# Performance work log

Hardware: AMD Instinct MI355X
Metric: run time of the kernel (lower is better)

Reference implementation:

```python
import jax, jax.numpy as jnp
import numpy as np


def _dense_image_warp(image, flow):
    """Faithful port of tfa.image.dense_image_warp (bilinear, edge-clamped).

    output[b, y, x, c] = image[b, y - flow[b,y,x,0], x - flow[b,y,x,1], c]
    with bilinear interpolation; floor indices clipped to [0, size-2] and
    alphas clipped to [0, 1], matching TFA's interpolate_bilinear.
    """
    B, H, W, C = image.shape
    gy = jnp.arange(H, dtype=flow.dtype)[None, :, None]  # [1,H,1]
    gx = jnp.arange(W, dtype=flow.dtype)[None, None, :]  # [1,1,W]
    qy = gy - flow[..., 0]  # [B,H,W] query y coords
    qx = gx - flow[..., 1]  # [B,H,W] query x coords

    y0f = jnp.clip(jnp.floor(qy), 0.0, H - 2)
    x0f = jnp.clip(jnp.floor(qx), 0.0, W - 2)
    ay = jnp.clip(qy - y0f, 0.0, 1.0)[..., None]  # [B,H,W,1]
    ax = jnp.clip(qx - x0f, 0.0, 1.0)[..., None]
    y0 = y0f.astype(jnp.int32)
    x0 = x0f.astype(jnp.int32)
    y1 = y0 + 1
    x1 = x0 + 1

    b_idx = jnp.arange(B, dtype=jnp.int32)[:, None, None]  # [B,1,1]
    tl = image[b_idx, y0, x0]  # [B,H,W,C]
    tr = image[b_idx, y0, x1]
    bl = image[b_idx, y1, x0]
    br = image[b_idx, y1, x1]

    top = tl + ax * (tr - tl)
    bot = bl + ax * (br - bl)
    return top + ay * (bot - top)


def setup_inputs() -> dict:
    key = jax.random.key(0)
    k0, k1, k2, k3 = jax.random.split(key, 4)
    B, H, W = 16, 512, 512
    return {
        "frame_0": jax.random.uniform(k0, (B, H, W, 3), dtype=jnp.float32),
        "frame_1": jax.random.uniform(k1, (B, H, W, 3), dtype=jnp.float32),
        "f_01": jax.random.normal(k2, (B, H, W, 2), dtype=jnp.float32),
        "f_10": jax.random.normal(k3, (B, H, W, 2), dtype=jnp.float32),
    }


def reference(frame_0, frame_1, f_01, f_10):
    # WarpingOutput: [backwarp(frame_0, f_10), backwarp(frame_1, f_01)]
    return (_dense_image_warp(frame_0, f_10), _dense_image_warp(frame_1, f_01))
```

## Files before the change

kernel.cpp:

```cpp
#include <hip/hip_runtime.h>

#define BB 16
#define HH 512
#define WW 512
#define TH 16
#define TW 64
#define HALO 8
#define SR 33
#define SC 80
#define ROWQ (SC / 4)
#define NUNIT (SR * ROWQ)
#define NPIX (BB * HH * WW)

typedef float vf4 __attribute__((ext_vector_type(4)));
typedef unsigned int u32;
typedef u32 vu4 __attribute__((ext_vector_type(4)));
typedef u32 vu2 __attribute__((ext_vector_type(2)));

__device__ __forceinline__ u32 cvt_pk_bf16(float lo, float hi) {
    u32 r;
    asm("v_cvt_pk_bf16_f32 %0, %1, %2" : "=v"(r) : "v"(lo), "v"(hi));
    return r;
}
__device__ __forceinline__ float bf_lo(u32 w) { return __uint_as_float(w << 16); }
__device__ __forceinline__ float bf_hi(u32 w) { return __uint_as_float(w & 0xffff0000u); }

__global__ __launch_bounds__(256, 7) void warp2_kernel(
    const float* __restrict__ frame0,
    const float* __restrict__ frame1,
    const float* __restrict__ f01,
    const float* __restrict__ f10,
    float* __restrict__ out)
{
    __shared__ vu2 plds[SR * SC];

    const int bid = blockIdx.x;
    const int gt  = (bid & 7) * 1024 + (bid >> 3);
    const int which = gt >> 12;
    const int b     = (gt >> 8) & 15;
    const int tt    = gt & 255;
    const int ty    = (tt >> 3) * TH;
    const int tx    = (tt & 7) * TW;

    const float* __restrict__ img  = which ? frame1 : frame0;
    const float* __restrict__ flow = which ? f01    : f10;

    const int r0 = min(max(ty - HALO, 0), HH - SR);
    const int c0 = min(max(tx - HALO, 0), WW - SC);

    const int tid = threadIdx.x;

    const int r  = tid >> 4;
    const int q  = tid & 15;
    const int y  = ty + r;
    const int xq = tx + (q << 2);
    const size_t pixbase = (size_t)(b * HH + y) * WW + xq;
    const vf4 fl0 = __builtin_nontemporal_load(reinterpret_cast<const vf4*>(flow + 2 * pixbase));
    const vf4 fl1 = __builtin_nontemporal_load(reinterpret_cast<const vf4*>(flow + 2 * pixbase + 4));

    #pragma unroll
    for (int it = 0; it < 3; ++it) {
        const int s = tid + (it << 8);
        if (it < 2 || s < NUNIT) {
            const int row = s / ROWQ;
            const int u   = s - row * ROWQ;
            const float* g = img + ((size_t)((b * HH + r0 + row) * WW + c0 + (u << 2))) * 3;
            const vf4 a0 = *reinterpret_cast<const vf4*>(g);
            const vf4 a1 = *reinterpret_cast<const vf4*>(g + 4);
            const vf4 a2 = *reinterpret_cast<const vf4*>(g + 8);
            const vu4 w0 = { cvt_pk_bf16(a0.x, a0.y), cvt_pk_bf16(a0.z, 0.0f),
                             cvt_pk_bf16(a0.w, a1.x), cvt_pk_bf16(a1.y, 0.0f) };
            const vu4 w1 = { cvt_pk_bf16(a1.z, a1.w), cvt_pk_bf16(a2.x, 0.0f),
                             cvt_pk_bf16(a2.y, a2.z), cvt_pk_bf16(a2.w, 0.0f) };
            const int base = row * SC + (u << 2);
            *reinterpret_cast<vu4*>(&plds[base])     = w0;
            *reinterpret_cast<vu4*>(&plds[base + 2]) = w1;
        }
    }
    __syncthreads();

    float res[12];
    #pragma unroll
    for (int s = 0; s < 4; ++s) {
        const float dy = (s == 0) ? fl0.x : (s == 1) ? fl0.z : (s == 2) ? fl1.x : fl1.z;
        const float dx = (s == 0) ? fl0.y : (s == 1) ? fl0.w : (s == 2) ? fl1.y : fl1.w;
        const int xs = xq + s;

        const float qy = (float)y  - dy;
        const float qx = (float)xs - dx;
        const float y0f = fminf(fmaxf(floorf(qy), 0.0f), (float)(HH - 2));
        const float x0f = fminf(fmaxf(floorf(qx), 0.0f), (float)(WW - 2));
        const float ay = fminf(fmaxf(qy - y0f, 0.0f), 1.0f);
        const float ax = fminf(fmaxf(qx - x0f, 0.0f), 1.0f);
        const int y0 = (int)y0f;
        const int x0 = (int)x0f;

        float tl0, tl1, tl2, tr0, tr1, tr2, bl0, bl1, bl2, br0, br1, br2;
        if (y0 >= r0 && y0 < r0 + SR - 1 && x0 >= c0 && x0 < c0 + SC - 1) {
            const int o = (y0 - r0) * SC + (x0 - c0);
            const vu2 tl = plds[o];      const vu2 tr = plds[o + 1];
            const vu2 bl = plds[o + SC]; const vu2 br = plds[o + SC + 1];
            tl0 = bf_lo(tl.x); tl1 = bf_hi(tl.x); tl2 = bf_lo(tl.y);
            tr0 = bf_lo(tr.x); tr1 = bf_hi(tr.x); tr2 = bf_lo(tr.y);
            bl0 = bf_lo(bl.x); bl1 = bf_hi(bl.x); bl2 = bf_lo(bl.y);
            br0 = bf_lo(br.x); br1 = bf_hi(br.x); br2 = bf_lo(br.y);
        } else {
            const float* rowt = img + ((size_t)((b * HH + y0) * WW + x0)) * 3;
            const float* rowb = rowt + WW * 3;
            const float3 tl = *reinterpret_cast<const float3*>(rowt);
            const float3 tr = *reinterpret_cast<const float3*>(rowt + 3);
            const float3 bl = *reinterpret_cast<const float3*>(rowb);
            const float3 br = *reinterpret_cast<const float3*>(rowb + 3);
            tl0 = tl.x; tl1 = tl.y; tl2 = tl.z;
            tr0 = tr.x; tr1 = tr.y; tr2 = tr.z;
            bl0 = bl.x; bl1 = bl.y; bl2 = bl.z;
            br0 = br.x; br1 = br.y; br2 = br.z;
        }

        const float t0 = fmaf(ax, tr0 - tl0, tl0);
        const float t1 = fmaf(ax, tr1 - tl1, tl1);
        const float t2 = fmaf(ax, tr2 - tl2, tl2);
        const float q0 = fmaf(ax, br0 - bl0, bl0);
        const float q1 = fmaf(ax, br1 - bl1, bl1);
        const float q2 = fmaf(ax, br2 - bl2, bl2);
        res[3 * s + 0] = fmaf(ay, q0 - t0, t0);
        res[3 * s + 1] = fmaf(ay, q1 - t1, t1);
        res[3 * s + 2] = fmaf(ay, q2 - t2, t2);
    }

    float* o = out + 3 * (((size_t)which) * NPIX + pixbase);
    const vf4 s0 = {res[0], res[1], res[2],  res[3]};
    const vf4 s1 = {res[4], res[5], res[6],  res[7]};
    const vf4 s2 = {res[8], res[9], res[10], res[11]};
    *reinterpret_cast<vf4*>(o)     = s0;
    *reinterpret_cast<vf4*>(o + 4) = s1;
    *reinterpret_cast<vf4*>(o + 8) = s2;
}

extern "C" void kernel_launch(void* const* d_in, const int* in_sizes, int n_in,
                              void* d_out, int out_size, void* d_ws, size_t ws_size,
                              hipStream_t stream) {
    const float* frame0 = (const float*)d_in[0];
    const float* frame1 = (const float*)d_in[1];
    const float* f01    = (const float*)d_in[2];
    const float* f10    = (const float*)d_in[3];
    float* out = (float*)d_out;

    warp2_kernel<<<8192, 256, 0, stream>>>(frame0, frame1, f01, f10, out);
}
```

Before: 57.45 us.

## Double tile height, 8 pixels per thread, pad LDS stride

Doubles the output tile height to 32 rows so the staged halo region (49x80) is amortized over more output pixels. Each thread now handles 8 pixels, halving the block count. The shared-memory row stride is padded to 81 to reduce bank conflicts, which forces the staging stores to be split into four 8-byte writes. Occupancy hint drops to 5 blocks per CU because of the larger LDS footprint and register use.

```diff
diff --git a/kernel.cpp b/kernel.cpp
--- a/kernel.cpp
+++ b/kernel.cpp
@@ -3,18 +3,18 @@
 #define BB 16
 #define HH 512
 #define WW 512
-#define TH 16
+#define TH 32
 #define TW 64
 #define HALO 8
-#define SR 33
+#define SR 49
 #define SC 80
+#define SSTRIDE 81
 #define ROWQ (SC / 4)
 #define NUNIT (SR * ROWQ)
 #define NPIX (BB * HH * WW)
 
 typedef float vf4 __attribute__((ext_vector_type(4)));
 typedef unsigned int u32;
-typedef u32 vu4 __attribute__((ext_vector_type(4)));
 typedef u32 vu2 __attribute__((ext_vector_type(2)));
 
 __device__ __forceinline__ u32 cvt_pk_bf16(float lo, float hi) {
@@ -25,20 +25,20 @@
 __device__ __forceinline__ float bf_lo(u32 w) { return __uint_as_float(w << 16); }
 __device__ __forceinline__ float bf_hi(u32 w) { return __uint_as_float(w & 0xffff0000u); }
 
-__global__ __launch_bounds__(256, 7) void warp2_kernel(
+__global__ __launch_bounds__(256, 5) void warp2_kernel(
     const float* __restrict__ frame0,
     const float* __restrict__ frame1,
     const float* __restrict__ f01,
     const float* __restrict__ f10,
     float* __restrict__ out)
 {
-    __shared__ vu2 plds[SR * SC];
+    __shared__ vu2 plds[SR * SSTRIDE];
 
     const int bid = blockIdx.x;
-    const int gt  = (bid & 7) * 1024 + (bid >> 3);
-    const int which = gt >> 12;
-    const int b     = (gt >> 8) & 15;
-    const int tt    = gt & 255;
+    const int gt  = (bid & 7) * 512 + (bid >> 3);
+    const int which = gt >> 11;
+    const int b     = (gt >> 7) & 15;
+    const int tt    = gt & 127;
     const int ty    = (tt >> 3) * TH;
     const int tx    = (tt & 7) * TW;
 
@@ -50,40 +50,42 @@
 
     const int tid = threadIdx.x;
 
-    const int r  = tid >> 4;
-    const int q  = tid & 15;
+    const int r  = tid >> 3;
+    const int k  = tid & 7;
     const int y  = ty + r;
-    const int xq = tx + (q << 2);
+    const int xq = tx + (k << 3);
     const size_t pixbase = (size_t)(b * HH + y) * WW + xq;
-    const vf4 fl0 = __builtin_nontemporal_load(reinterpret_cast<const vf4*>(flow + 2 * pixbase));
-    const vf4 fl1 = __builtin_nontemporal_load(reinterpret_cast<const vf4*>(flow + 2 * pixbase + 4));
+
+    const vf4 fA = __builtin_nontemporal_load(reinterpret_cast<const vf4*>(flow + 2 * pixbase));
+    const vf4 fB = __builtin_nontemporal_load(reinterpret_cast<const vf4*>(flow + 2 * pixbase + 4));
+    const vf4 fC = __builtin_nontemporal_load(reinterpret_cast<const vf4*>(flow + 2 * pixbase + 8));
+    const vf4 fD = __builtin_nontemporal_load(reinterpret_cast<const vf4*>(flow + 2 * pixbase + 12));
 
     #pragma unroll
-    for (int it = 0; it < 3; ++it) {
+    for (int it = 0; it < 4; ++it) {
         const int s = tid + (it << 8);
-        if (it < 2 || s < NUNIT) {
+        if (it < 3 || s < NUNIT) {
             const int row = s / ROWQ;
             const int u   = s - row * ROWQ;
             const float* g = img + ((size_t)((b * HH + r0 + row) * WW + c0 + (u << 2))) * 3;
             const vf4 a0 = *reinterpret_cast<const vf4*>(g);
             const vf4 a1 = *reinterpret_cast<const vf4*>(g + 4);
             const vf4 a2 = *reinterpret_cast<const vf4*>(g + 8);
-            const vu4 w0 = { cvt_pk_bf16(a0.x, a0.y), cvt_pk_bf16(a0.z, 0.0f),
-                             cvt_pk_bf16(a0.w, a1.x), cvt_pk_bf16(a1.y, 0.0f) };
-            const vu4 w1 = { cvt_pk_bf16(a1.z, a1.w), cvt_pk_bf16(a2.x, 0.0f),
-                             cvt_pk_bf16(a2.y, a2.z), cvt_pk_bf16(a2.w, 0.0f) };
-            const int base = row * SC + (u << 2);
-            *reinterpret_cast<vu4*>(&plds[base])     = w0;
-            *reinterpret_cast<vu4*>(&plds[base + 2]) = w1;
+            const int base = row * SSTRIDE + (u << 2);
+            plds[base]     = (vu2){ cvt_pk_bf16(a0.x, a0.y), cvt_pk_bf16(a0.z, 0.0f) };
+            plds[base + 1] = (vu2){ cvt_pk_bf16(a0.w, a1.x), cvt_pk_bf16(a1.y, 0.0f) };
+            plds[base + 2] = (vu2){ cvt_pk_bf16(a1.z, a1.w), cvt_pk_bf16(a2.x, 0.0f) };
+            plds[base + 3] = (vu2){ cvt_pk_bf16(a2.y, a2.z), cvt_pk_bf16(a2.w, 0.0f) };
         }
     }
     __syncthreads();
 
-    float res[12];
+    float res[24];
     #pragma unroll
-    for (int s = 0; s < 4; ++s) {
-        const float dy = (s == 0) ? fl0.x : (s == 1) ? fl0.z : (s == 2) ? fl1.x : fl1.z;
-        const float dx = (s == 0) ? fl0.y : (s == 1) ? fl0.w : (s == 2) ? fl1.y : fl1.w;
+    for (int s = 0; s < 8; ++s) {
+        const vf4 fv = (s < 2) ? fA : (s < 4) ? fB : (s < 6) ? fC : fD;
+        const float dy = (s & 1) ? fv.z : fv.x;
+        const float dx = (s & 1) ? fv.w : fv.y;
         const int xs = xq + s;
 
         const float qy = (float)y  - dy;
@@ -97,9 +99,9 @@
 
         float tl0, tl1, tl2, tr0, tr1, tr2, bl0, bl1, bl2, br0, br1, br2;
         if (y0 >= r0 && y0 < r0 + SR - 1 && x0 >= c0 && x0 < c0 + SC - 1) {
-            const int o = (y0 - r0) * SC + (x0 - c0);
-            const vu2 tl = plds[o];      const vu2 tr = plds[o + 1];
-            const vu2 bl = plds[o + SC]; const vu2 br = plds[o + SC + 1];
+            const int o = (y0 - r0) * SSTRIDE + (x0 - c0);
+            const vu2 tl = plds[o];            const vu2 tr = plds[o + 1];
+            const vu2 bl = plds[o + SSTRIDE];  const vu2 br = plds[o + SSTRIDE + 1];
             tl0 = bf_lo(tl.x); tl1 = bf_hi(tl.x); tl2 = bf_lo(tl.y);
             tr0 = bf_lo(tr.x); tr1 = bf_hi(tr.x); tr2 = bf_lo(tr.y);
             bl0 = bf_lo(bl.x); bl1 = bf_hi(bl.x); bl2 = bf_lo(bl.y);
@@ -129,12 +131,11 @@
     }
 
     float* o = out + 3 * (((size_t)which) * NPIX + pixbase);
-    const vf4 s0 = {res[0], res[1], res[2],  res[3]};
-    const vf4 s1 = {res[4], res[5], res[6],  res[7]};
-    const vf4 s2 = {res[8], res[9], res[10], res[11]};
-    *reinterpret_cast<vf4*>(o)     = s0;
-    *reinterpret_cast<vf4*>(o + 4) = s1;
-    *reinterpret_cast<vf4*>(o + 8) = s2;
+    #pragma unroll
+    for (int v = 0; v < 6; ++v) {
+        const vf4 sv = {res[4 * v], res[4 * v + 1], res[4 * v + 2], res[4 * v + 3]};
+        *reinterpret_cast<vf4*>(o + 4 * v) = sv;
+    }
 }
 
 extern "C" void kernel_launch(void* const* d_in, const int* in_sizes, int n_in,
@@ -146,5 +147,5 @@
     const float* f10    = (const float*)d_in[3];
     float* out = (float*)d_out;
 
-    warp2_kernel<<<8192, 256, 0, stream>>>(frame0, frame1, f01, f10, out);
+    warp2_kernel<<<4096, 256, 0, stream>>>(frame0, frame1, f01, f10, out);
 }
```

After: 128.9 us. +124.4%, slower.
